# Kernel optimization log

Hardware: AMD Instinct MI355X
Metric: run time of the kernel (lower is better)

## Reference

```python
import jax, jax.numpy as jnp
import numpy as np

H, W = 512, 1024          # ERP panorama resolution
K = 15                    # neighbour_nb (degree_max)
N = H * W                 # pixel count (norm_const)
GAMMA = 0.1
MULTIPLIER = 1.0


def erp_dirs():
    """Unit ray directions for an equirectangular grid, shape [3, H, W].
    (EquirecGrid.to_xyz convention: pixel-centered lon/lat spherical rays.)"""
    lat = (0.5 - (jnp.arange(H, dtype=jnp.float32) + 0.5) / H) * jnp.pi       # [H]
    lon = ((jnp.arange(W, dtype=jnp.float32) + 0.5) / W - 0.5) * 2.0 * jnp.pi  # [W]
    lat = lat[:, None]
    lon = lon[None, :]
    x = jnp.cos(lat) * jnp.sin(lon)
    y = jnp.broadcast_to(jnp.sin(lat), (H, W))
    z = jnp.cos(lat) * jnp.cos(lon)
    return jnp.stack([x, y, z], axis=0)  # [3,H,W]


def setup_inputs() -> dict:
    key = jax.random.key(0)
    k1, k2, k3, k4 = jax.random.split(key, 4)
    sig1 = jax.random.uniform(k1, (1, 1, H, W), dtype=jnp.float32) * 10.0 + 0.1  # depth > 0
    sig2 = jax.random.normal(k2, (1, 3, H, W), dtype=jnp.float32)                # normals
    weights = jax.random.uniform(k3, (K, N), dtype=jnp.float32)                  # graph edge weights
    neighbours = jax.random.randint(k4, (K, N), 0, N, dtype=jnp.int64)           # neighbour pixel ids
    return {"sig1": sig1, "sig2": sig2, "weights": weights, "neighbours": neighbours}


def reference(sig1, sig2, weights, neighbours):
    dirs = erp_dirs()                       # [3,H,W]
    p = (sig1[0, 0] * dirs).reshape(3, -1)  # cam points, [3,N]
    n = sig2[0].reshape(3, -1)              # normals,    [3,N]

    pn = jnp.sum(p * n, axis=0)             # <p_i, n_i>, [N]
    p_nb = p[:, neighbours]                 # gathered neighbour points,  [3,K,N]
    n_nb = n[:, neighbours]                 # gathered neighbour normals, [3,K,N]

    # aux1[k,i] = <p_i, n_i> - <p_{nb(k,i)}, n_i>
    aux1 = pn[None, :] - jnp.sum(p_nb * n[:, None, :], axis=0)   # [K,N]
    # aux2[k,i] = || n_i - n_{nb(k,i)} ||_2
    aux2 = jnp.linalg.norm(n[:, None, :] - n_nb, axis=0)         # [K,N]

    term1 = jnp.linalg.norm(aux1 * weights, axis=0).sum()        # norm over K, sum over pixels
    term2 = (aux2 * weights).sum()
    loss = (term1 + GAMMA * term2) / N
    return MULTIPLIER * loss
```

## Files before the change

### kernel.cpp

```cpp
#include <hip/hip_runtime.h>
#include <hip/hip_fp16.h>
#include <math.h>

#define HH 512
#define WW 1024
#define NPIX (HH * WW)
#define KK 15
#define GAMMA 0.1f
#define MULTIPLIER 1.0f


__device__ inline unsigned int pack2f(float a, float b) {
  __half2 h = __floats2half2_rn(a, b);
  return *(unsigned int*)&h;
}
__device__ inline float2 up2(unsigned int u) {
  __half2 h = *(__half2*)&u;
  return __half22float2(h);
}

__global__ __launch_bounds__(256) void prep_kernel(
    const float* __restrict__ sig1,
    const float* __restrict__ sig2,
    uint4* __restrict__ pack,
    float* __restrict__ acc) {
  int i = blockIdx.x * 256 + threadIdx.x;
  if (i == 0) acc[0] = 0.0f;

  int h = i >> 10;
  int w = i & (WW - 1);
  const float PI = 3.14159265358979323846f;
  float lat = (0.5f - (h + 0.5f) * (1.0f / HH)) * PI;
  float lon = ((w + 0.5f) * (1.0f / WW) - 0.5f) * (2.0f * PI);
  float sla = __sinf(lat), cla = __cosf(lat);
  float slo = __sinf(lon), clo = __cosf(lon);
  float dx = cla * slo;
  float dy = sla;
  float dz = cla * clo;

  float s = sig1[i];
  float nx = sig2[i];
  float ny = sig2[NPIX + i];
  float nz = sig2[2 * NPIX + i];

  float px = s * dx, py = s * dy, pz = s * dz;
  float pn = px * nx + py * ny + pz * nz;

  uint4 u;
  u.x = pack2f(px, py);
  u.y = pack2f(pz, nx);
  u.z = pack2f(ny, nz);
  u.w = __float_as_uint(pn);
  pack[i] = u;
}

__global__ __launch_bounds__(256) void main_kernel(
    const uint4* __restrict__ pack,
    const float* __restrict__ weights,
    const int* __restrict__ nb,
    float* __restrict__ acc) {
  int i = blockIdx.x * 256 + threadIdx.x;

  int j[KK];
#pragma unroll
  for (int k = 0; k < KK; ++k) j[k] = nb[k * NPIX + i];

  uint4 g[KK];
#pragma unroll
  for (int k = 0; k < KK; ++k) g[k] = pack[j[k]];

  float wv[KK];
#pragma unroll
  for (int k = 0; k < KK; ++k) wv[k] = weights[k * NPIX + i];

  uint4 c = pack[i];
  float2 cy = up2(c.y), cz = up2(c.z);
  float nix = cy.y, niy = cz.x, niz = cz.y;
  float pn = __uint_as_float(c.w);

  float sq = 0.0f, t2 = 0.0f;
#pragma unroll
  for (int k = 0; k < KK; ++k) {
    float2 gx = up2(g[k].x);
    float2 gy = up2(g[k].y);
    float2 gz = up2(g[k].z);
    float aux1 = pn - (gx.x * nix + gx.y * niy + gy.x * niz);
    float ddx = nix - gy.y, ddy = niy - gz.x, ddz = niz - gz.y;
    float aux2 = sqrtf(ddx * ddx + ddy * ddy + ddz * ddz);
    float aw = aux1 * wv[k];
    sq += aw * aw;
    t2 += aux2 * wv[k];
  }
  float local = sqrtf(sq) + GAMMA * t2;

  for (int off = 32; off > 0; off >>= 1)
    local += __shfl_down(local, off, 64);

  __shared__ float smem[4];
  int lane = threadIdx.x & 63;
  int wid = threadIdx.x >> 6;
  if (lane == 0) smem[wid] = local;
  __syncthreads();
  if (threadIdx.x == 0) {
    float s = smem[0] + smem[1] + smem[2] + smem[3];
    atomicAdd(acc, s);
  }
}

__global__ void fin_kernel(const float* __restrict__ acc, float* __restrict__ out) {
  if (threadIdx.x == 0 && blockIdx.x == 0)
    out[0] = MULTIPLIER * acc[0] * (1.0f / (float)NPIX);
}

extern "C" void kernel_launch(void* const* d_in, const int* in_sizes, int n_in,
                              void* d_out, int out_size, void* d_ws, size_t ws_size,
                              hipStream_t stream) {
  const float* sig1 = (const float*)d_in[0];
  const float* sig2 = (const float*)d_in[1];
  const float* wts  = (const float*)d_in[2];
  const int*   nb   = (const int*)d_in[3];
  float* out = (float*)d_out;

  float* acc = (float*)d_ws;
  uint4* pack = (uint4*)((char*)d_ws + 256);

  int blocks = NPIX / 256;
  hipLaunchKernelGGL(prep_kernel, dim3(blocks), dim3(256), 0, stream, sig1, sig2, pack, acc);
  hipLaunchKernelGGL(main_kernel, dim3(blocks), dim3(256), 0, stream, pack, wts, nb, acc);
  hipLaunchKernelGGL(fin_kernel, dim3(1), dim3(64), 0, stream, acc, out);
}
```

Measured before the change: 174.5 us.

## Shrink packed gather record to 8 bytes and recompute ray directions per neighbour

Each pixel's packed record now holds only depth and normal in half precision (8 bytes instead of 16), and the ERP ray direction is recomputed from the neighbour index inside the main kernel with fast sin/cos. This halves the random-gather footprint at the cost of extra transcendental math per edge. The neighbour-index and weight streams use nontemporal loads. The separate finalize kernel is replaced by a last-block-done counter that writes the output. Storing depth as fp16 instead of fp16 products slightly changes rounding.

```diff
diff --git a/kernel.cpp b/kernel.cpp
--- a/kernel.cpp
+++ b/kernel.cpp
@@ -19,73 +19,76 @@
   return __half22float2(h);
 }
 
-__global__ __launch_bounds__(256) void prep_kernel(
-    const float* __restrict__ sig1,
-    const float* __restrict__ sig2,
-    uint4* __restrict__ pack,
-    float* __restrict__ acc) {
-  int i = blockIdx.x * 256 + threadIdx.x;
-  if (i == 0) acc[0] = 0.0f;
-
-  int h = i >> 10;
-  int w = i & (WW - 1);
+__device__ inline void erp_dir(int idx, float& dx, float& dy, float& dz) {
+  int h = idx >> 10;
+  int w = idx & (WW - 1);
   const float PI = 3.14159265358979323846f;
   float lat = (0.5f - (h + 0.5f) * (1.0f / HH)) * PI;
   float lon = ((w + 0.5f) * (1.0f / WW) - 0.5f) * (2.0f * PI);
   float sla = __sinf(lat), cla = __cosf(lat);
   float slo = __sinf(lon), clo = __cosf(lon);
-  float dx = cla * slo;
-  float dy = sla;
-  float dz = cla * clo;
+  dx = cla * slo;
+  dy = sla;
+  dz = cla * clo;
+}
 
-  float s = sig1[i];
+__global__ __launch_bounds__(256) void prep_kernel(
+    const float* __restrict__ sig1,
+    const float* __restrict__ sig2,
+    uint2* __restrict__ pack,
+    float* __restrict__ acc,
+    unsigned* __restrict__ done) {
+  int i = blockIdx.x * 256 + threadIdx.x;
+  if (i == 0) { acc[0] = 0.0f; done[0] = 0u; }
+
+  float s  = sig1[i];
   float nx = sig2[i];
   float ny = sig2[NPIX + i];
   float nz = sig2[2 * NPIX + i];
 
-  float px = s * dx, py = s * dy, pz = s * dz;
-  float pn = px * nx + py * ny + pz * nz;
-
-  uint4 u;
-  u.x = pack2f(px, py);
-  u.y = pack2f(pz, nx);
-  u.z = pack2f(ny, nz);
-  u.w = __float_as_uint(pn);
+  uint2 u;
+  u.x = pack2f(s, nx);
+  u.y = pack2f(ny, nz);
   pack[i] = u;
 }
 
 __global__ __launch_bounds__(256) void main_kernel(
-    const uint4* __restrict__ pack,
+    const uint2* __restrict__ pack,
     const float* __restrict__ weights,
     const int* __restrict__ nb,
-    float* __restrict__ acc) {
+    float* __restrict__ acc,
+    unsigned* __restrict__ done,
+    float* __restrict__ out) {
   int i = blockIdx.x * 256 + threadIdx.x;
+
+  float dix, diy, diz;
+  erp_dir(i, dix, diy, diz);
+  uint2 c = pack[i];
+  float2 c0 = up2(c.x), c1 = up2(c.y);
+  float si = c0.x, nix = c0.y, niy = c1.x, niz = c1.y;
+  float pn = si * (dix * nix + diy * niy + diz * niz);
 
   int j[KK];
 #pragma unroll
-  for (int k = 0; k < KK; ++k) j[k] = nb[k * NPIX + i];
+  for (int k = 0; k < KK; ++k) j[k] = __builtin_nontemporal_load(&nb[k * NPIX + i]);
 
-  uint4 g[KK];
+  uint2 g[KK];
 #pragma unroll
   for (int k = 0; k < KK; ++k) g[k] = pack[j[k]];
 
   float wv[KK];
 #pragma unroll
-  for (int k = 0; k < KK; ++k) wv[k] = weights[k * NPIX + i];
-
-  uint4 c = pack[i];
-  float2 cy = up2(c.y), cz = up2(c.z);
-  float nix = cy.y, niy = cz.x, niz = cz.y;
-  float pn = __uint_as_float(c.w);
+  for (int k = 0; k < KK; ++k) wv[k] = __builtin_nontemporal_load(&weights[k * NPIX + i]);
 
   float sq = 0.0f, t2 = 0.0f;
 #pragma unroll
   for (int k = 0; k < KK; ++k) {
-    float2 gx = up2(g[k].x);
-    float2 gy = up2(g[k].y);
-    float2 gz = up2(g[k].z);
-    float aux1 = pn - (gx.x * nix + gx.y * niy + gy.x * niz);
-    float ddx = nix - gy.y, ddy = niy - gz.x, ddz = niz - gz.y;
+    float djx, djy, djz;
+    erp_dir(j[k], djx, djy, djz);
+    float2 g0 = up2(g[k].x), g1 = up2(g[k].y);
+    float sj = g0.x, njx = g0.y, njy = g1.x, njz = g1.y;
+    float aux1 = pn - sj * (djx * nix + djy * niy + djz * niz);
+    float ddx = nix - njx, ddy = niy - njy, ddz = niz - njz;
     float aux2 = sqrtf(ddx * ddx + ddy * ddy + ddz * ddz);
     float aw = aux1 * wv[k];
     sq += aw * aw;
@@ -104,12 +107,14 @@
   if (threadIdx.x == 0) {
     float s = smem[0] + smem[1] + smem[2] + smem[3];
     atomicAdd(acc, s);
+    __threadfence();
+    unsigned t = atomicAdd(done, 1u);
+    if (t == gridDim.x - 1) {
+      __threadfence();
+      float a = *((volatile float*)acc);
+      out[0] = MULTIPLIER * a * (1.0f / (float)NPIX);
+    }
   }
-}
-
-__global__ void fin_kernel(const float* __restrict__ acc, float* __restrict__ out) {
-  if (threadIdx.x == 0 && blockIdx.x == 0)
-    out[0] = MULTIPLIER * acc[0] * (1.0f / (float)NPIX);
 }
 
 extern "C" void kernel_launch(void* const* d_in, const int* in_sizes, int n_in,
@@ -121,11 +126,11 @@
   const int*   nb   = (const int*)d_in[3];
   float* out = (float*)d_out;
 
-  float* acc = (float*)d_ws;
-  uint4* pack = (uint4*)((char*)d_ws + 256);
+  float*    acc  = (float*)d_ws;
+  unsigned* done = (unsigned*)d_ws + 1;
+  uint2*    pack = (uint2*)((char*)d_ws + 256);
 
   int blocks = NPIX / 256;
-  hipLaunchKernelGGL(prep_kernel, dim3(blocks), dim3(256), 0, stream, sig1, sig2, pack, acc);
-  hipLaunchKernelGGL(main_kernel, dim3(blocks), dim3(256), 0, stream, pack, wts, nb, acc);
-  hipLaunchKernelGGL(fin_kernel, dim3(1), dim3(64), 0, stream, acc, out);
+  hipLaunchKernelGGL(prep_kernel, dim3(blocks), dim3(256), 0, stream, sig1, sig2, pack, acc, done);
+  hipLaunchKernelGGL(main_kernel, dim3(blocks), dim3(256), 0, stream, pack, wts, nb, acc, done, out);
 }
```

After: 230.3 us. 32.0% more time.
